# Kernel optimization log

Measured on AMD Instinct MI355X. Metric: run time of the kernel, lower is better.

Reference implementation:

```python
import jax, jax.numpy as jnp
import numpy as np

B, C, H, W, K = 16, 64, 256, 256, 3

def setup_inputs() -> dict:
    key = jax.random.key(0)
    ks = jax.random.split(key, 3)
    x = jax.random.normal(ks[0], (B, C, H, W), dtype=jnp.float32)
    # ReDistribution params
    rd_k = jnp.ones((1, C, 1, 1), jnp.float32)
    rd_b = jnp.zeros((1, C, 1, 1), jnp.float32)
    # Spectral binary activation beta
    beta = jnp.ones((1,), jnp.float32)
    # HardBinaryConv real-valued latent weights (Conv2d default init scale)
    fan_in = C * K * K
    bound = 1.0 / np.sqrt(fan_in)
    conv_w = jax.random.uniform(ks[1], (C, C, K, K), jnp.float32, -bound, bound)
    # RPReLU params
    pr_bias0 = jnp.zeros((1, C, 1, 1), jnp.float32)
    prelu_w = jnp.full((C,), 0.25, jnp.float32)
    pr_bias1 = jnp.zeros((1, C, 1, 1), jnp.float32)
    return {"x": x, "rd_k": rd_k, "rd_b": rd_b, "beta": beta,
            "conv_w": conv_w, "pr_bias0": pr_bias0, "prelu_w": prelu_w,
            "pr_bias1": pr_bias1}

def _ste(hard, soft):
    # straight-through estimator: forward=hard, backward grads flow via soft
    return jax.lax.stop_gradient(hard - soft) + soft

def reference(x, rd_k, rd_b, beta, conv_w, pr_bias0, prelu_w, pr_bias1):
    sg = jax.lax.stop_gradient
    # ReDistribution
    out = x * rd_k + rd_b
    # Spectral binary activation with tanh STE
    out = _ste(jnp.sign(out), jnp.tanh(out * beta))
    # HardBinaryConv: per-output-channel mean |w| scaling, sign binarize, clip STE
    scaling = sg(jnp.mean(jnp.abs(conv_w), axis=(1, 2, 3), keepdims=True))  # [C,1,1,1]
    bw = _ste(scaling * jnp.sign(conv_w), jnp.clip(conv_w, -1.0, 1.0))
    y = jax.lax.conv_general_dilated(
        out, bw, window_strides=(1, 1), padding=((1, 1), (1, 1)),
        dimension_numbers=("NCHW", "OIHW", "NCHW"))
    # RPReLU: bias0 -> per-channel PReLU -> bias1
    y = y + pr_bias0
    y = jnp.where(y >= 0, y, prelu_w[None, :, None, None] * y)
    y = y + pr_bias1
    return y + x
```

## Files before the change

kernel.cpp:

```cpp
#include <hip/hip_runtime.h>
#include <cstdint>
#include <cstddef>

#define Bn 16
#define Cn 64
#define Hn 256
#define Wn 256
#define HWn (Hn * Wn)
#define TH 8
#define TW 128
#define ROWS (TH + 2)
#define COLS (TW + 2)
#define NBLK (Bn * (Hn / TH) * (Wn / TW))

typedef unsigned long long u64;
typedef u64   u64x2 __attribute__((ext_vector_type(2)));
typedef float f32x4 __attribute__((ext_vector_type(4)));

__global__ __launch_bounds__(64) void pack_weights(const float* __restrict__ w,
                                                   const float* __restrict__ b0g,
                                                   const float* __restrict__ pwg,
                                                   const float* __restrict__ b1g,
                                                   u64* __restrict__ wbits,
                                                   float4* __restrict__ par,
                                                   int* __restrict__ corrx) {
    const int co = blockIdx.x;
    const int ci = threadIdx.x;
    const float* wp = w + ((size_t)co * Cn + ci) * 9;
    float v[9];
    float asum = 0.f;
    #pragma unroll
    for (int t = 0; t < 9; ++t) { v[t] = wp[t]; asum += fabsf(v[t]); }
    u64 m[9];
    #pragma unroll
    for (int t = 0; t < 9; ++t) m[t] = __ballot(v[t] > 0.f);
    #pragma unroll
    for (int off = 32; off; off >>= 1) asum += __shfl_xor(asum, off);
    if (ci == 0) {
        int c[9];
        #pragma unroll
        for (int t = 0; t < 9; ++t) {
            wbits[co * 9 + t] = m[t];
            c[t] = 64 - 2 * (int)__popcll(m[t]);
        }
        int* cx = corrx + co * 8;
        cx[0] = c[0] + c[1] + c[2];
        cx[1] = c[6] + c[7] + c[8];
        cx[2] = c[0] + c[3] + c[6];
        cx[3] = c[2] + c[5] + c[8];
        cx[4] = c[0]; cx[5] = c[2];
        cx[6] = c[6]; cx[7] = c[8];
        par[co] = make_float4(asum * (1.f / (Cn * 9)), b0g[co], pwg[co], b1g[co]);
    }
}

__global__ __launch_bounds__(256) void fused(const float* __restrict__ x,
                                             const float* __restrict__ rdk,
                                             const float* __restrict__ rdb,
                                             const u64* __restrict__ wbits,
                                             const float4* __restrict__ par,
                                             const int* __restrict__ corrx,
                                             float* __restrict__ out) {
    __shared__ __align__(16) u64 s_a[ROWS][COLS];
    __shared__ float2 s_rd[Cn];

    const int tid = threadIdx.x;
    const int bid     = blockIdx.x;
    const int logical = (bid & 7) * (NBLK / 8) + (bid >> 3);
    const int n   = logical >> 6;
    const int rem = logical & 63;
    const int h0  = (rem >> 1) * TH;
    const int w0  = (rem & 1) * TW;

    if (tid < Cn) s_rd[tid] = make_float2(rdk[tid], rdb[tid]);
    __syncthreads();

    const float* xn = x + (size_t)n * Cn * HWn;
    #pragma unroll
    for (int it = 0; it < 3; ++it) {
        const int task = tid + it * 256;
        if (task < 640) {
            const int r = task >> 6;
            const int k = task & 63;
            const int gh = h0 - 1 + r;
            const int gw = w0 + 2 * k;
            u64 b0 = 0, b1 = 0;
            if (gh >= 0 && gh < Hn) {
                const float* xp = xn + (size_t)gh * Wn + gw;
                #pragma unroll 8
                for (int ci = 0; ci < Cn; ++ci) {
                    const float2 kb = s_rd[ci];
                    const float2 v = *reinterpret_cast<const float2*>(xp + (size_t)ci * HWn);
                    const u64 bit = 1ull << ci;
                    if (fmaf(v.x, kb.x, kb.y) > 0.f) b0 |= bit;
                    if (fmaf(v.y, kb.x, kb.y) > 0.f) b1 |= bit;
                }
            }
            s_a[r][1 + 2 * k] = b0;
            s_a[r][2 + 2 * k] = b1;
        } else if (task < 660) {
            const int t2 = task - 640;
            const int r = t2 >> 1;
            const int side = t2 & 1;
            const int gh = h0 - 1 + r;
            const int gw = side ? (w0 + TW) : (w0 - 1);
            u64 b = 0;
            if (gh >= 0 && gh < Hn && gw >= 0 && gw < Wn) {
                const float* xp = xn + (size_t)gh * Wn + gw;
                #pragma unroll 8
                for (int ci = 0; ci < Cn; ++ci) {
                    const float2 kb = s_rd[ci];
                    if (fmaf(xp[(size_t)ci * HWn], kb.x, kb.y) > 0.f) b |= 1ull << ci;
                }
            }
            s_a[r][side ? (COLS - 1) : 0] = b;
        }
    }
    __syncthreads();

    const int r  = tid >> 5;
    const int c0 = (tid & 31) * 4;

    u64 A[3][6];
    #pragma unroll
    for (int dh = 0; dh < 3; ++dh)
        #pragma unroll
        for (int q = 0; q < 3; ++q) {
            const u64x2 t = *reinterpret_cast<const u64x2*>(&s_a[r + dh][c0 + 2 * q]);
            A[dh][2 * q]     = t.x;
            A[dh][2 * q + 1] = t.y;
        }
    __syncthreads();
    float4* parL = reinterpret_cast<float4*>(&s_a[0][0]);
    if (tid < Cn) parL[tid] = par[tid];
    __syncthreads();

    const int gw0  = w0 + c0;
    const int h    = h0 + r;
    const int htop = (h == 0), hbot = (h == Hn - 1);
    const int wl   = (gw0 == 0), wr = (gw0 + 3 == Wn - 1);
    const int need = htop | hbot | wl | wr;

    const float* xp = x   + (size_t)n * Cn * HWn + (size_t)h * Wn + gw0;
    float*       op = out + (size_t)n * Cn * HWn + (size_t)h * Wn + gw0;

    f32x4 xa = *reinterpret_cast<const f32x4*>(xp);
    #pragma unroll 2
    for (int co = 0; co < Cn; ++co) {
        const int nco = (co < Cn - 1) ? co + 1 : co;
        const f32x4 xa_n = *reinterpret_cast<const f32x4*>(xp + (size_t)nco * HWn);

        const u64* wb = wbits + co * 9;
        int isum[4];
        #pragma unroll
        for (int p = 0; p < 4; ++p) {
            int acc = 0;
            #pragma unroll
            for (int dh = 0; dh < 3; ++dh) {
                acc += (int)__popcll(A[dh][p]     ^ wb[dh * 3]);
                acc += (int)__popcll(A[dh][p + 1] ^ wb[dh * 3 + 1]);
                acc += (int)__popcll(A[dh][p + 2] ^ wb[dh * 3 + 2]);
            }
            isum[p] = 576 - 2 * acc;
        }

        if (need) {
            const int* cx = corrx + co * 8;
            const int sb = (htop ? cx[0] : 0) + (hbot ? cx[1] : 0);
            #pragma unroll
            for (int p = 0; p < 4; ++p) isum[p] -= sb;
            if (wl) isum[0] -= cx[2] - (htop ? cx[4] : 0) - (hbot ? cx[6] : 0);
            if (wr) isum[3] -= cx[3] - (htop ? cx[5] : 0) - (hbot ? cx[7] : 0);
        }

        const float4 p4 = parL[co];
        f32x4 o;
        #pragma unroll
        for (int j = 0; j < 4; ++j) {
            float y = fmaf(p4.x, (float)isum[j], p4.y);
            y = (y >= 0.f) ? y : y * p4.z;
            o[j] = y + p4.w + xa[j];
        }
        __builtin_nontemporal_store(o, reinterpret_cast<f32x4*>(op + (size_t)co * HWn));
        xa = xa_n;
    }
}

extern "C" void kernel_launch(void* const* d_in, const int* in_sizes, int n_in,
                              void* d_out, int out_size, void* d_ws, size_t ws_size,
                              hipStream_t stream) {
    const float* x      = (const float*)d_in[0];
    const float* rd_k   = (const float*)d_in[1];
    const float* rd_b   = (const float*)d_in[2];
    const float* conv_w = (const float*)d_in[4];
    const float* pb0    = (const float*)d_in[5];
    const float* pw     = (const float*)d_in[6];
    const float* pb1    = (const float*)d_in[7];
    float* out = (float*)d_out;

    uint8_t* ws = (uint8_t*)d_ws;
    u64*    wbits = (u64*)ws;
    float4* par   = (float4*)(ws + 4608);
    int*    corrx = (int*)(ws + 4608 + 1024);

    pack_weights<<<Cn, 64, 0, stream>>>(conv_w, pb0, pw, pb1, wbits, par, corrx);
    fused<<<NBLK, 256, 0, stream>>>(x, rd_k, rd_b, wbits, par, corrx, out);
}
```

Measured before the change: 161.5 us.

## Widen binarization loads to float4, deepen prefetch, drop LDS param staging

The halo binarization phase now has each thread load four consecutive floats per channel, which halves the number of tasks and load instructions. The per-channel parameters are read straight from global/constant memory rather than staged through LDS, which removes two block barriers. The epilogue prefetches x two channels ahead and launch bounds now request 4 blocks per CU. In exchange, registers per thread may rise, and the halo load is less parallel because only 320 threads do the interior work.

Result: no change. 164.4 us (+1.7%).

```diff
diff --git a/kernel.cpp b/kernel.cpp
--- a/kernel.cpp
+++ b/kernel.cpp
@@ -14,7 +14,6 @@
 #define NBLK (Bn * (Hn / TH) * (Wn / TW))
 
 typedef unsigned long long u64;
-typedef u64   u64x2 __attribute__((ext_vector_type(2)));
 typedef float f32x4 __attribute__((ext_vector_type(4)));
 
 __global__ __launch_bounds__(64) void pack_weights(const float* __restrict__ w,
@@ -54,13 +53,13 @@
     }
 }
 
-__global__ __launch_bounds__(256) void fused(const float* __restrict__ x,
-                                             const float* __restrict__ rdk,
-                                             const float* __restrict__ rdb,
-                                             const u64* __restrict__ wbits,
-                                             const float4* __restrict__ par,
-                                             const int* __restrict__ corrx,
-                                             float* __restrict__ out) {
+__global__ __launch_bounds__(256, 4) void fused(const float* __restrict__ x,
+                                                const float* __restrict__ rdk,
+                                                const float* __restrict__ rdb,
+                                                const u64* __restrict__ wbits,
+                                                const float4* __restrict__ par,
+                                                const int* __restrict__ corrx,
+                                                float* __restrict__ out) {
     __shared__ __align__(16) u64 s_a[ROWS][COLS];
     __shared__ float2 s_rd[Cn];
 
@@ -76,30 +75,32 @@
     __syncthreads();
 
     const float* xn = x + (size_t)n * Cn * HWn;
-    #pragma unroll
-    for (int it = 0; it < 3; ++it) {
-        const int task = tid + it * 256;
-        if (task < 640) {
-            const int r = task >> 6;
-            const int k = task & 63;
+    for (int task = tid; task < 340; task += 256) {
+        if (task < 320) {
+            const int r = task >> 5;
+            const int q = task & 31;
             const int gh = h0 - 1 + r;
-            const int gw = w0 + 2 * k;
-            u64 b0 = 0, b1 = 0;
+            const int gw = w0 + 4 * q;
+            u64 b0 = 0, b1 = 0, b2 = 0, b3 = 0;
             if (gh >= 0 && gh < Hn) {
                 const float* xp = xn + (size_t)gh * Wn + gw;
                 #pragma unroll 8
                 for (int ci = 0; ci < Cn; ++ci) {
                     const float2 kb = s_rd[ci];
-                    const float2 v = *reinterpret_cast<const float2*>(xp + (size_t)ci * HWn);
+                    const f32x4 v = *reinterpret_cast<const f32x4*>(xp + (size_t)ci * HWn);
                     const u64 bit = 1ull << ci;
                     if (fmaf(v.x, kb.x, kb.y) > 0.f) b0 |= bit;
                     if (fmaf(v.y, kb.x, kb.y) > 0.f) b1 |= bit;
+                    if (fmaf(v.z, kb.x, kb.y) > 0.f) b2 |= bit;
+                    if (fmaf(v.w, kb.x, kb.y) > 0.f) b3 |= bit;
                 }
             }
-            s_a[r][1 + 2 * k] = b0;
-            s_a[r][2 + 2 * k] = b1;
-        } else if (task < 660) {
-            const int t2 = task - 640;
+            s_a[r][1 + 4 * q] = b0;
+            s_a[r][2 + 4 * q] = b1;
+            s_a[r][3 + 4 * q] = b2;
+            s_a[r][4 + 4 * q] = b3;
+        } else {
+            const int t2 = task - 320;
             const int r = t2 >> 1;
             const int side = t2 & 1;
             const int gh = h0 - 1 + r;
@@ -125,15 +126,13 @@
     #pragma unroll
     for (int dh = 0; dh < 3; ++dh)
         #pragma unroll
-        for (int q = 0; q < 3; ++q) {
-            const u64x2 t = *reinterpret_cast<const u64x2*>(&s_a[r + dh][c0 + 2 * q]);
-            A[dh][2 * q]     = t.x;
-            A[dh][2 * q + 1] = t.y;
-        }
-    __syncthreads();
-    float4* parL = reinterpret_cast<float4*>(&s_a[0][0]);
-    if (tid < Cn) parL[tid] = par[tid];
-    __syncthreads();
+        for (int j = 0; j < 6; ++j)
+            A[dh][j] = s_a[r + dh][c0 + j];
+    #pragma unroll
+    for (int dh = 0; dh < 3; ++dh)
+        #pragma unroll
+        for (int j = 0; j < 6; ++j)
+            asm volatile("" : "+v"(A[dh][j]));
 
     const int gw0  = w0 + c0;
     const int h    = h0 + r;
@@ -144,14 +143,9 @@
     const float* xp = x   + (size_t)n * Cn * HWn + (size_t)h * Wn + gw0;
     float*       op = out + (size_t)n * Cn * HWn + (size_t)h * Wn + gw0;
 
-    f32x4 xa = *reinterpret_cast<const f32x4*>(xp);
-    #pragma unroll 2
-    for (int co = 0; co < Cn; ++co) {
-        const int nco = (co < Cn - 1) ? co + 1 : co;
-        const f32x4 xa_n = *reinterpret_cast<const f32x4*>(xp + (size_t)nco * HWn);
-
+    auto conv1 = [&](int co, const f32x4& xv) {
         const u64* wb = wbits + co * 9;
-        int isum[4];
+        int is[4];
         #pragma unroll
         for (int p = 0; p < 4; ++p) {
             int acc = 0;
@@ -161,28 +155,38 @@
                 acc += (int)__popcll(A[dh][p + 1] ^ wb[dh * 3 + 1]);
                 acc += (int)__popcll(A[dh][p + 2] ^ wb[dh * 3 + 2]);
             }
-            isum[p] = 576 - 2 * acc;
-        }
-
+            is[p] = 576 - 2 * acc;
+        }
         if (need) {
             const int* cx = corrx + co * 8;
             const int sb = (htop ? cx[0] : 0) + (hbot ? cx[1] : 0);
             #pragma unroll
-            for (int p = 0; p < 4; ++p) isum[p] -= sb;
-            if (wl) isum[0] -= cx[2] - (htop ? cx[4] : 0) - (hbot ? cx[6] : 0);
-            if (wr) isum[3] -= cx[3] - (htop ? cx[5] : 0) - (hbot ? cx[7] : 0);
-        }
-
-        const float4 p4 = parL[co];
+            for (int p = 0; p < 4; ++p) is[p] -= sb;
+            if (wl) is[0] -= cx[2] - (htop ? cx[4] : 0) - (hbot ? cx[6] : 0);
+            if (wr) is[3] -= cx[3] - (htop ? cx[5] : 0) - (hbot ? cx[7] : 0);
+        }
+        const float4 p4 = par[co];
         f32x4 o;
         #pragma unroll
         for (int j = 0; j < 4; ++j) {
-            float y = fmaf(p4.x, (float)isum[j], p4.y);
+            float y = fmaf(p4.x, (float)is[j], p4.y);
             y = (y >= 0.f) ? y : y * p4.z;
-            o[j] = y + p4.w + xa[j];
+            o[j] = y + p4.w + xv[j];
         }
         __builtin_nontemporal_store(o, reinterpret_cast<f32x4*>(op + (size_t)co * HWn));
-        xa = xa_n;
+    };
+
+    f32x4 xva = *reinterpret_cast<const f32x4*>(xp);
+    f32x4 xvb = *reinterpret_cast<const f32x4*>(xp + HWn);
+    for (int co = 0; co < Cn; co += 2) {
+        const int pfa = (co + 2 < Cn) ? co + 2 : co;
+        const f32x4 na = *reinterpret_cast<const f32x4*>(xp + (size_t)pfa * HWn);
+        conv1(co, xva);
+        xva = na;
+        const int pfb = (co + 3 < Cn) ? co + 3 : co + 1;
+        const f32x4 nb = *reinterpret_cast<const f32x4*>(xp + (size_t)pfb * HWn);
+        conv1(co + 1, xvb);
+        xvb = nb;
     }
 }
 
```
